# Performance work log

Hardware: AMD Instinct MI355X
Metric: run time of the kernel (lower is better)

The kernel has to match this reference:

```python
import jax, jax.numpy as jnp
import numpy as np

DN = ('NCDHW', 'DHWIO', 'NCDHW')


def _w(key, cin, cout):
    # kernel_size=3 in 3D, Minkowski-style fan-in scaling, no bias
    scale = 1.0 / np.sqrt(cin * 27)
    return jax.random.normal(key, (3, 3, 3, cin, cout), dtype=jnp.float32) * scale


def setup_inputs() -> dict:
    key = jax.random.key(0)
    ks = jax.random.split(key, 7)
    x = jax.random.normal(ks[0], (1, 1024, 4, 4, 4), dtype=jnp.float32)
    chans = [(1024, 512), (512, 256), (256, 128), (128, 64), (64, 32), (32, 1)]
    ws = {f'w{i+1}': _w(ks[i + 1], ci, co) for i, (ci, co) in enumerate(chans)}
    return {'x': x, **ws}


def _ct(x, w, stride):
    # conv-transpose, kernel 3, SAME padding: stride 2 doubles resolution,
    # stride 1 preserves it (dense analog of Minkowski generative transpose conv)
    return jax.lax.conv_transpose(x, w, strides=(stride, stride, stride),
                                  padding='SAME', dimension_numbers=DN)


def reference(x, w1, w2, w3, w4, w5, w6):
    h = jax.nn.relu(_ct(x, w1, 2))   # 1024 -> 512, 4^3 -> 8^3
    h = jax.nn.relu(_ct(h, w2, 1))   # 512 -> 256
    h = jax.nn.relu(_ct(h, w3, 2))   # 256 -> 128, 8^3 -> 16^3
    h = jax.nn.relu(_ct(h, w4, 1))   # 128 -> 64
    h = jax.nn.relu(_ct(h, w5, 2))   # 64 -> 32, 16^3 -> 32^3
    return _ct(h, w6, 1)             # 32 -> 1, no final ReLU
```

## Files before the change

kernel.cpp:

```cpp
#include <hip/hip_runtime.h>

typedef _Float16 half8 __attribute__((ext_vector_type(8)));
typedef _Float16 half4v __attribute__((ext_vector_type(4)));
typedef float floatx4 __attribute__((ext_vector_type(4)));


__global__ __launch_bounds__(256) void pad_x_k(const float* __restrict__ X,
                                               _Float16* __restrict__ P) {
  int idx = blockIdx.x * 256 + threadIdx.x;
  if (idx >= 125 * 1024) return;
  int c = idx & 1023;
  int r = idx >> 10;
  int px = r % 5, py = (r / 5) % 5, pz = r / 25;
  float v = 0.f;
  if (px >= 1 && py >= 1 && pz >= 1)
    v = X[c * 64 + (pz - 1) * 16 + (py - 1) * 4 + (px - 1)];
  P[idx] = (_Float16)v;
}

template <int S, int PS, int C, int RELU>
__global__ __launch_bounds__(256) void pad_k(const float* __restrict__ I,
                                             _Float16* __restrict__ P) {
  constexpr int TOT = PS * PS * PS * C;
  int idx = blockIdx.x * 256 + threadIdx.x;
  if (idx >= TOT) return;
  int c = idx % C;
  int r = idx / C;
  int px = r % PS;
  int ry = r / PS;
  int py = ry % PS, pz = ry / PS;
  int sx = px - 1, sy = py - 1, sz = pz - 1;
  float v = 0.f;
  if (sx >= 0 && sx < S && sy >= 0 && sy < S && sz >= 0 && sz < S) {
    v = I[(size_t)((sz * S + sy) * S + sx) * C + c];
    if (RELU) v = fmaxf(v, 0.f);
  }
  P[idx] = (_Float16)v;
}

__global__ __launch_bounds__(256) void wt_k(
    const float* __restrict__ w1, const float* __restrict__ w2,
    const float* __restrict__ w3, const float* __restrict__ w4,
    const float* __restrict__ w5, _Float16* __restrict__ t1,
    _Float16* __restrict__ t2, _Float16* __restrict__ t3,
    _Float16* __restrict__ t4, _Float16* __restrict__ t5) {
  int b = blockIdx.x;
  const float* W;
  _Float16* T;
  int cin, cout;
  if (b < 13824)      { W = w1; T = t1; cin = 1024; cout = 512; }
  else if (b < 17280) { b -= 13824; W = w2; T = t2; cin = 512; cout = 256; }
  else if (b < 18144) { b -= 17280; W = w3; T = t3; cin = 256; cout = 128; }
  else if (b < 18360) { b -= 18144; W = w4; T = t4; cin = 128; cout = 64; }
  else                { b -= 18360; W = w5; T = t5; cin = 64;  cout = 32; }
  const int citiles = cin >> 5;
  const int per_tap = (cout >> 5) * citiles;
  const int tap = b / per_tap;
  const int r = b - tap * per_tap;
  const int cot = r / citiles, cit = r - cot * citiles;

  __shared__ float tile[32][33];
  const int t = threadIdx.x;
  const int rr = t >> 3, c4 = (t & 7) * 4;
  const float* src =
      W + ((size_t)(tap * cin + cit * 32 + rr)) * cout + cot * 32 + c4;
  float4 v = *(const float4*)src;
  tile[rr][c4] = v.x; tile[rr][c4 + 1] = v.y;
  tile[rr][c4 + 2] = v.z; tile[rr][c4 + 3] = v.w;
  __syncthreads();
  half4v h;
  h[0] = (_Float16)tile[c4 + 0][rr];
  h[1] = (_Float16)tile[c4 + 1][rr];
  h[2] = (_Float16)tile[c4 + 2][rr];
  h[3] = (_Float16)tile[c4 + 3][rr];
  *(half4v*)(T + ((size_t)(tap * cout + cot * 32 + rr)) * cin + cit * 32 + c4) = h;
}

template <int CICHUNK, int CIN, int COUT, int NTILE, int STRIDE2, int SOUTU,
          int TZ, int PS, int USE_ATOMIC>
__global__ __launch_bounds__(256) void conv_mfma_k(
    const _Float16* __restrict__ P, const _Float16* __restrict__ Wt,
    float* __restrict__ O) {
  constexpr int M = TZ * 16;
  constexpr int MTZ = SOUTU / TZ;
  constexpr int MTXY = SOUTU / 4;
  constexpr int MT3 = MTZ * MTXY * MTXY;
  constexpr int KB = 32;
  constexpr int KP = KB + 8;
  constexpr int S = STRIDE2 ? 2 * SOUTU : SOUTU;

  __shared__ __align__(16) _Float16 As[M][KP];
  __shared__ __align__(16) _Float16 Bs[NTILE][KP];

  int bx = blockIdx.x;
  int cls = 0;
  if (STRIDE2) { cls = bx / MT3; bx -= cls * MT3; }
  const int clz = (cls >> 2) & 1, cly = (cls >> 1) & 1, clx = cls & 1;
  const int u0z = (bx / (MTXY * MTXY)) * TZ;
  const int u0y = ((bx / MTXY) % MTXY) * 4;
  const int u0x = (bx % MTXY) * 4;
  const int n_base = blockIdx.y * NTILE;
  const int ci_base = blockIdx.z * CICHUNK;

  const int t = threadIdx.x;
  const int lane = t & 63;
  const int wave = t >> 6;

  const int skq = t & 3;
  const int sp = t >> 2;
  const int spx = sp & 3, spy = (sp >> 2) & 3, spz = sp >> 4;
  const int aoff0 = ((spz * PS + spy) * PS + spx) * CIN;
  const int aoff1 = (((spz + 4) * PS + spy) * PS + spx) * CIN;

  const int m0w = (NTILE == 64) ? (wave >> 1) * 32 : wave * 32;
  const int n0w = (NTILE == 64) ? (wave & 1) * 32 : 0;
  const int fr = lane & 15;
  const int fq = lane >> 4;

  floatx4 acc[2][2];
#pragma unroll
  for (int i = 0; i < 2; i++)
#pragma unroll
    for (int j = 0; j < 2; j++) acc[i][j] = {0.f, 0.f, 0.f, 0.f};

  const int cz = STRIDE2 ? (clz ? 1 : 2) : 3;
  const int cy = STRIDE2 ? (cly ? 1 : 2) : 3;
  const int cx = STRIDE2 ? (clx ? 1 : 2) : 3;

  for (int iz = 0; iz < cz; iz++) {
    const int toz = STRIDE2 ? (clz ? 1 : iz) : iz;
    const int wz  = STRIDE2 ? (clz ? 1 : 2 * iz) : iz;
    for (int iy = 0; iy < cy; iy++) {
      const int toy = STRIDE2 ? (cly ? 1 : iy) : iy;
      const int wy  = STRIDE2 ? (cly ? 1 : 2 * iy) : iy;
      for (int ix = 0; ix < cx; ix++) {
        const int tox = STRIDE2 ? (clx ? 1 : ix) : ix;
        const int wx  = STRIDE2 ? (clx ? 1 : 2 * ix) : ix;
        const _Float16* Pb = P +
            (size_t)(((u0z + toz) * PS + (u0y + toy)) * PS + (u0x + tox)) * CIN +
            ci_base;
        const _Float16* Wb = Wt +
            ((size_t)((wz * 3 + wy) * 3 + wx) * COUT + n_base) * CIN + ci_base;
        for (int kb = 0; kb < CICHUNK / KB; kb++) {
          const int ko = kb * KB + skq * 8;
          *(half8*)&As[sp][skq * 8] = *(const half8*)(Pb + aoff0 + ko);
          if (M == 128)
            *(half8*)&As[sp + 64][skq * 8] = *(const half8*)(Pb + aoff1 + ko);
          if (NTILE == 64 || sp < NTILE)
            *(half8*)&Bs[sp][skq * 8] =
                *(const half8*)(Wb + (size_t)sp * CIN + ko);
          __syncthreads();
          half8 a0 = *(const half8*)&As[m0w + fr][fq * 8];
          half8 a1 = *(const half8*)&As[m0w + 16 + fr][fq * 8];
          half8 b0 = *(const half8*)&Bs[n0w + fr][fq * 8];
          half8 b1 = *(const half8*)&Bs[n0w + 16 + fr][fq * 8];
          acc[0][0] = __builtin_amdgcn_mfma_f32_16x16x32_f16(a0, b0, acc[0][0], 0, 0, 0);
          acc[0][1] = __builtin_amdgcn_mfma_f32_16x16x32_f16(a0, b1, acc[0][1], 0, 0, 0);
          acc[1][0] = __builtin_amdgcn_mfma_f32_16x16x32_f16(a1, b0, acc[1][0], 0, 0, 0);
          acc[1][1] = __builtin_amdgcn_mfma_f32_16x16x32_f16(a1, b1, acc[1][1], 0, 0, 0);
          __syncthreads();
        }
      }
    }
  }

#pragma unroll
  for (int i = 0; i < 2; i++) {
#pragma unroll
    for (int r = 0; r < 4; r++) {
      const int m = m0w + i * 16 + fq * 4 + r;
      const int mz = m >> 4, my = (m >> 2) & 3, mx = m & 3;
      int oz, oy, ox;
      if (STRIDE2) {
        oz = 2 * (u0z + mz) + clz;
        oy = 2 * (u0y + my) + cly;
        ox = 2 * (u0x + mx) + clx;
      } else {
        oz = u0z + mz;
        oy = u0y + my;
        ox = u0x + mx;
      }
      float* obase = O + (size_t)((oz * S + oy) * S + ox) * COUT + n_base + n0w;
#pragma unroll
      for (int j = 0; j < 2; j++) {
        float* o = obase + j * 16 + fr;
        if (USE_ATOMIC) atomicAdd(o, acc[i][j][r]);
        else *o = acc[i][j][r];
      }
    }
  }
}

__global__ __launch_bounds__(256) void conv6_k(const _Float16* __restrict__ P,
                                               const float* __restrict__ W6,
                                               float* __restrict__ O) {
  __shared__ __align__(16) float w[864];
  for (int i = threadIdx.x; i < 864; i += 256) w[i] = W6[i];
  __syncthreads();
  int idx = blockIdx.x * 256 + threadIdx.x;
  int x = idx & 31, y = (idx >> 5) & 31, z = idx >> 10;
  float a = 0.f;
  for (int dz = 0; dz < 3; dz++)
    for (int dy = 0; dy < 3; dy++)
      for (int dx = 0; dx < 3; dx++) {
        const _Float16* p =
            P + (size_t)(((z + dz) * 34 + (y + dy)) * 34 + (x + dx)) * 32;
        const float* ww = &w[((dz * 3 + dy) * 3 + dx) * 32];
#pragma unroll
        for (int c = 0; c < 32; c += 8) {
          half8 pv = *(const half8*)&p[c];
#pragma unroll
          for (int u = 0; u < 8; u++) a += (float)pv[u] * ww[c + u];
        }
      }
  O[idx] = a;
}

extern "C" void kernel_launch(void* const* d_in, const int* in_sizes, int n_in,
                              void* d_out, int out_size, void* d_ws,
                              size_t ws_size, hipStream_t stream) {
  const float* x  = (const float*)d_in[0];
  const float* w1 = (const float*)d_in[1];
  const float* w2 = (const float*)d_in[2];
  const float* w3 = (const float*)d_in[3];
  const float* w4 = (const float*)d_in[4];
  const float* w5 = (const float*)d_in[5];
  const float* w6 = (const float*)d_in[6];
  float* out = (float*)d_out;

  float* O1 = (float*)d_ws;
  float* O2 = O1 + 262144;
  float* O3 = O2 + 131072;
  float* O4 = O3 + 524288;
  float* O5 = O4 + 262144;
  _Float16* P1 = (_Float16*)(O5 + 1048576);
  _Float16* P2 = P1 + 128000;
  _Float16* P3 = P2 + 512000;
  _Float16* P4 = P3 + 186624;
  _Float16* P5 = P4 + 746496;
  _Float16* P6 = P5 + 314432;
  _Float16* T1 = P6 + 1257728;
  _Float16* T2 = T1 + 14155776;
  _Float16* T3 = T2 + 3538944;
  _Float16* T4 = T3 + 884736;
  _Float16* T5 = T4 + 221184;

  wt_k<<<18414, 256, 0, stream>>>(w1, w2, w3, w4, w5, T1, T2, T3, T4, T5);
  hipMemsetAsync(O1, 0, (262144 + 131072 + 524288 + 262144) * sizeof(float),
                 stream);

  pad_x_k<<<500, 256, 0, stream>>>(x, P1);
  conv_mfma_k<256, 1024, 512, 64, 1, 4, 4, 5, 1>
      <<<dim3(8, 8, 4), 256, 0, stream>>>(P1, T1, O1);
  pad_k<8, 10, 512, 1><<<2000, 256, 0, stream>>>(O1, P2);
  conv_mfma_k<64, 512, 256, 64, 0, 8, 4, 10, 1>
      <<<dim3(8, 4, 8), 256, 0, stream>>>(P2, T2, O2);
  pad_k<8, 9, 256, 1><<<729, 256, 0, stream>>>(O2, P3);
  conv_mfma_k<128, 256, 128, 64, 1, 8, 4, 9, 1>
      <<<dim3(64, 2, 2), 256, 0, stream>>>(P3, T3, O3);
  pad_k<16, 18, 128, 1><<<2916, 256, 0, stream>>>(O3, P4);
  conv_mfma_k<32, 128, 64, 64, 0, 16, 4, 18, 1>
      <<<dim3(64, 1, 4), 256, 0, stream>>>(P4, T4, O4);
  pad_k<16, 17, 64, 1><<<1229, 256, 0, stream>>>(O4, P5);
  conv_mfma_k<64, 64, 32, 32, 1, 16, 8, 17, 0>
      <<<dim3(256, 1, 1), 256, 0, stream>>>(P5, T5, O5);
  pad_k<32, 34, 32, 1><<<4913, 256, 0, stream>>>(O5, P6);
  conv6_k<<<128, 256, 0, stream>>>(P6, w6, out);

  (void)in_sizes; (void)n_in; (void)out_size; (void)ws_size;
}
```

Measured before the change: 238.2 us.

## Read fp32 weights directly in conv, prefetch next tile, fuse last pad

Drops the separate weight transpose/convert kernel. Each conv now loads fp32 weights in their original DHWIO layout straight from global memory and converts them to fp16 while writing shared memory. The main loop is flattened over taps and K-blocks with register double-buffering, so the next tile's loads overlap the current MFMA step. Layer 5 writes ReLU'd fp16 output directly into the padded buffer, removing one pad kernel. Split-K factors change for layers 1–3. The trade-off is reading fp32 weights, twice the bytes and with strided per-thread loads, and more atomics from the larger split-K.

```diff
diff --git a/kernel.cpp b/kernel.cpp
--- a/kernel.cpp
+++ b/kernel.cpp
@@ -38,56 +38,20 @@
   P[idx] = (_Float16)v;
 }
 
-__global__ __launch_bounds__(256) void wt_k(
-    const float* __restrict__ w1, const float* __restrict__ w2,
-    const float* __restrict__ w3, const float* __restrict__ w4,
-    const float* __restrict__ w5, _Float16* __restrict__ t1,
-    _Float16* __restrict__ t2, _Float16* __restrict__ t3,
-    _Float16* __restrict__ t4, _Float16* __restrict__ t5) {
-  int b = blockIdx.x;
-  const float* W;
-  _Float16* T;
-  int cin, cout;
-  if (b < 13824)      { W = w1; T = t1; cin = 1024; cout = 512; }
-  else if (b < 17280) { b -= 13824; W = w2; T = t2; cin = 512; cout = 256; }
-  else if (b < 18144) { b -= 17280; W = w3; T = t3; cin = 256; cout = 128; }
-  else if (b < 18360) { b -= 18144; W = w4; T = t4; cin = 128; cout = 64; }
-  else                { b -= 18360; W = w5; T = t5; cin = 64;  cout = 32; }
-  const int citiles = cin >> 5;
-  const int per_tap = (cout >> 5) * citiles;
-  const int tap = b / per_tap;
-  const int r = b - tap * per_tap;
-  const int cot = r / citiles, cit = r - cot * citiles;
-
-  __shared__ float tile[32][33];
-  const int t = threadIdx.x;
-  const int rr = t >> 3, c4 = (t & 7) * 4;
-  const float* src =
-      W + ((size_t)(tap * cin + cit * 32 + rr)) * cout + cot * 32 + c4;
-  float4 v = *(const float4*)src;
-  tile[rr][c4] = v.x; tile[rr][c4 + 1] = v.y;
-  tile[rr][c4 + 2] = v.z; tile[rr][c4 + 3] = v.w;
-  __syncthreads();
-  half4v h;
-  h[0] = (_Float16)tile[c4 + 0][rr];
-  h[1] = (_Float16)tile[c4 + 1][rr];
-  h[2] = (_Float16)tile[c4 + 2][rr];
-  h[3] = (_Float16)tile[c4 + 3][rr];
-  *(half4v*)(T + ((size_t)(tap * cout + cot * 32 + rr)) * cin + cit * 32 + c4) = h;
-}
-
 template <int CICHUNK, int CIN, int COUT, int NTILE, int STRIDE2, int SOUTU,
-          int TZ, int PS, int USE_ATOMIC>
+          int TZ, int PS, int STORE_MODE>
 __global__ __launch_bounds__(256) void conv_mfma_k(
-    const _Float16* __restrict__ P, const _Float16* __restrict__ Wt,
-    float* __restrict__ O) {
+    const _Float16* __restrict__ P, const float* __restrict__ W,
+    void* __restrict__ Optr) {
   constexpr int M = TZ * 16;
   constexpr int MTZ = SOUTU / TZ;
   constexpr int MTXY = SOUTU / 4;
   constexpr int MT3 = MTZ * MTXY * MTXY;
   constexpr int KB = 32;
-  constexpr int KP = KB + 8;
+  constexpr int KP = 40;
+  constexpr int KBI = CICHUNK / KB;
   constexpr int S = STRIDE2 ? 2 * SOUTU : SOUTU;
+  constexpr int BJ = (NTILE == 64) ? 8 : 4;
 
   __shared__ __align__(16) _Float16 As[M][KP];
   __shared__ __align__(16) _Float16 Bs[NTILE][KP];
@@ -109,59 +73,102 @@
   const int skq = t & 3;
   const int sp = t >> 2;
   const int spx = sp & 3, spy = (sp >> 2) & 3, spz = sp >> 4;
-  const int aoff0 = ((spz * PS + spy) * PS + spx) * CIN;
-  const int aoff1 = (((spz + 4) * PS + spy) * PS + spx) * CIN;
+  const int aoffsp = ((spz * PS + spy) * PS + spx) * CIN + skq * 8;
+  const int aoffsp2 = (((spz + 4) * PS + spy) * PS + spx) * CIN + skq * 8;
+
+  const int nB = t & (NTILE - 1);
+  const int k0B = (t / NTILE) * BJ;
 
   const int m0w = (NTILE == 64) ? (wave >> 1) * 32 : wave * 32;
   const int n0w = (NTILE == 64) ? (wave & 1) * 32 : 0;
   const int fr = lane & 15;
   const int fq = lane >> 4;
 
-  floatx4 acc[2][2];
-#pragma unroll
-  for (int i = 0; i < 2; i++)
-#pragma unroll
-    for (int j = 0; j < 2; j++) acc[i][j] = {0.f, 0.f, 0.f, 0.f};
-
   const int cz = STRIDE2 ? (clz ? 1 : 2) : 3;
   const int cy = STRIDE2 ? (cly ? 1 : 2) : 3;
   const int cx = STRIDE2 ? (clx ? 1 : 2) : 3;
-
-  for (int iz = 0; iz < cz; iz++) {
+  const int ctaps = cz * cy * cx;
+  const int NIT = ctaps * KBI;
+  const int shx = STRIDE2 ? (clx ? 0 : 1) : 0;
+  const int shy = STRIDE2 ? (cly ? 0 : 1) : 0;
+
+  floatx4 acc[2][2];
+#pragma unroll
+  for (int i = 0; i < 2; i++)
+#pragma unroll
+    for (int j = 0; j < 2; j++) acc[i][j] = {0.f, 0.f, 0.f, 0.f};
+
+  half8 raA = {}, raB = {}, raA2 = {}, raB2 = {};
+  float bwv[BJ] = {}, bwv2[BJ] = {};
+
+  auto load_it = [&](int it, half8& A0, half8& A1, float* BW) {
+    int tap, kb;
+    if (KBI == 1) { tap = it; kb = 0; }
+    else { tap = it / KBI; kb = it - tap * KBI; }
+    int iz, iy, ix;
+    if (STRIDE2) {
+      const int shyx = shx + shy;
+      iz = tap >> shyx;
+      int rem = tap - (iz << shyx);
+      iy = rem >> shx;
+      ix = rem - (iy << shx);
+    } else {
+      iz = tap / 9;
+      int rem = tap - iz * 9;
+      iy = rem / 3;
+      ix = rem - iy * 3;
+    }
     const int toz = STRIDE2 ? (clz ? 1 : iz) : iz;
     const int wz  = STRIDE2 ? (clz ? 1 : 2 * iz) : iz;
-    for (int iy = 0; iy < cy; iy++) {
-      const int toy = STRIDE2 ? (cly ? 1 : iy) : iy;
-      const int wy  = STRIDE2 ? (cly ? 1 : 2 * iy) : iy;
-      for (int ix = 0; ix < cx; ix++) {
-        const int tox = STRIDE2 ? (clx ? 1 : ix) : ix;
-        const int wx  = STRIDE2 ? (clx ? 1 : 2 * ix) : ix;
-        const _Float16* Pb = P +
-            (size_t)(((u0z + toz) * PS + (u0y + toy)) * PS + (u0x + tox)) * CIN +
-            ci_base;
-        const _Float16* Wb = Wt +
-            ((size_t)((wz * 3 + wy) * 3 + wx) * COUT + n_base) * CIN + ci_base;
-        for (int kb = 0; kb < CICHUNK / KB; kb++) {
-          const int ko = kb * KB + skq * 8;
-          *(half8*)&As[sp][skq * 8] = *(const half8*)(Pb + aoff0 + ko);
-          if (M == 128)
-            *(half8*)&As[sp + 64][skq * 8] = *(const half8*)(Pb + aoff1 + ko);
-          if (NTILE == 64 || sp < NTILE)
-            *(half8*)&Bs[sp][skq * 8] =
-                *(const half8*)(Wb + (size_t)sp * CIN + ko);
-          __syncthreads();
-          half8 a0 = *(const half8*)&As[m0w + fr][fq * 8];
-          half8 a1 = *(const half8*)&As[m0w + 16 + fr][fq * 8];
-          half8 b0 = *(const half8*)&Bs[n0w + fr][fq * 8];
-          half8 b1 = *(const half8*)&Bs[n0w + 16 + fr][fq * 8];
-          acc[0][0] = __builtin_amdgcn_mfma_f32_16x16x32_f16(a0, b0, acc[0][0], 0, 0, 0);
-          acc[0][1] = __builtin_amdgcn_mfma_f32_16x16x32_f16(a0, b1, acc[0][1], 0, 0, 0);
-          acc[1][0] = __builtin_amdgcn_mfma_f32_16x16x32_f16(a1, b0, acc[1][0], 0, 0, 0);
-          acc[1][1] = __builtin_amdgcn_mfma_f32_16x16x32_f16(a1, b1, acc[1][1], 0, 0, 0);
-          __syncthreads();
-        }
+    const int toy = STRIDE2 ? (cly ? 1 : iy) : iy;
+    const int wy  = STRIDE2 ? (cly ? 1 : 2 * iy) : iy;
+    const int tox = STRIDE2 ? (clx ? 1 : ix) : ix;
+    const int wx  = STRIDE2 ? (clx ? 1 : 2 * ix) : ix;
+    const int kofs = ci_base + kb * KB;
+    const size_t pbase =
+        (size_t)(((u0z + toz) * PS + (u0y + toy)) * PS + (u0x + tox)) * CIN +
+        kofs;
+    A0 = *(const half8*)(P + pbase + aoffsp);
+    if (M == 128) A1 = *(const half8*)(P + pbase + aoffsp2);
+    const int wtap = (wz * 3 + wy) * 3 + wx;
+    const float* wb =
+        W + ((size_t)wtap * CIN + kofs + k0B) * COUT + n_base + nB;
+#pragma unroll
+    for (int j = 0; j < BJ; j++) BW[j] = wb[(size_t)j * COUT];
+  };
+
+  load_it(0, raA, raB, bwv);
+
+  for (int it = 0; it < NIT; ++it) {
+    *(half8*)&As[sp][skq * 8] = raA;
+    if (M == 128) *(half8*)&As[sp + 64][skq * 8] = raB;
+    {
+      half4v h0;
+#pragma unroll
+      for (int j = 0; j < 4; j++) h0[j] = (_Float16)bwv[j];
+      *(half4v*)&Bs[nB][k0B] = h0;
+      if (BJ == 8) {
+        half4v h1;
+#pragma unroll
+        for (int j = 0; j < 4; j++) h1[j] = (_Float16)bwv[4 + j];
+        *(half4v*)&Bs[nB][k0B + 4] = h1;
       }
     }
+    __syncthreads();
+    if (it + 1 < NIT) load_it(it + 1, raA2, raB2, bwv2);
+    half8 a0 = *(const half8*)&As[m0w + fr][fq * 8];
+    half8 a1 = *(const half8*)&As[m0w + 16 + fr][fq * 8];
+    half8 b0 = *(const half8*)&Bs[n0w + fr][fq * 8];
+    half8 b1 = *(const half8*)&Bs[n0w + 16 + fr][fq * 8];
+    acc[0][0] = __builtin_amdgcn_mfma_f32_16x16x32_f16(a0, b0, acc[0][0], 0, 0, 0);
+    acc[0][1] = __builtin_amdgcn_mfma_f32_16x16x32_f16(a0, b1, acc[0][1], 0, 0, 0);
+    acc[1][0] = __builtin_amdgcn_mfma_f32_16x16x32_f16(a1, b0, acc[1][0], 0, 0, 0);
+    acc[1][1] = __builtin_amdgcn_mfma_f32_16x16x32_f16(a1, b1, acc[1][1], 0, 0, 0);
+    __syncthreads();
+    raA = raA2;
+    raB = raB2;
+#pragma unroll
+    for (int j = 0; j < BJ; j++) bwv[j] = bwv2[j];
   }
 
 #pragma unroll
@@ -180,12 +187,21 @@
         oy = u0y + my;
         ox = u0x + mx;
       }
-      float* obase = O + (size_t)((oz * S + oy) * S + ox) * COUT + n_base + n0w;
-#pragma unroll
-      for (int j = 0; j < 2; j++) {
-        float* o = obase + j * 16 + fr;
-        if (USE_ATOMIC) atomicAdd(o, acc[i][j][r]);
-        else *o = acc[i][j][r];
+      if (STORE_MODE == 2) {
+        _Float16* o = (_Float16*)Optr +
+            (size_t)(((oz + 1) * (S + 2) + (oy + 1)) * (S + 2) + (ox + 1)) *
+                COUT + n_base + n0w;
+#pragma unroll
+        for (int j = 0; j < 2; j++)
+          o[j * 16 + fr] = (_Float16)fmaxf(acc[i][j][r], 0.f);
+      } else {
+        float* o = (float*)Optr +
+            (size_t)((oz * S + oy) * S + ox) * COUT + n_base + n0w;
+#pragma unroll
+        for (int j = 0; j < 2; j++) {
+          if (STORE_MODE == 1) atomicAdd(o + j * 16 + fr, acc[i][j][r]);
+          else o[j * 16 + fr] = acc[i][j][r];
+        }
       }
     }
   }
@@ -232,39 +248,31 @@
   float* O2 = O1 + 262144;
   float* O3 = O2 + 131072;
   float* O4 = O3 + 524288;
-  float* O5 = O4 + 262144;
-  _Float16* P1 = (_Float16*)(O5 + 1048576);
+  _Float16* P6 = (_Float16*)(O4 + 262144);
+  _Float16* P1 = P6 + 1257728;
   _Float16* P2 = P1 + 128000;
   _Float16* P3 = P2 + 512000;
   _Float16* P4 = P3 + 186624;
   _Float16* P5 = P4 + 746496;
-  _Float16* P6 = P5 + 314432;
-  _Float16* T1 = P6 + 1257728;
-  _Float16* T2 = T1 + 14155776;
-  _Float16* T3 = T2 + 3538944;
-  _Float16* T4 = T3 + 884736;
-  _Float16* T5 = T4 + 221184;
-
-  wt_k<<<18414, 256, 0, stream>>>(w1, w2, w3, w4, w5, T1, T2, T3, T4, T5);
-  hipMemsetAsync(O1, 0, (262144 + 131072 + 524288 + 262144) * sizeof(float),
+
+  hipMemsetAsync(d_ws, 0, 1179648 * sizeof(float) + 1257728 * sizeof(_Float16),
                  stream);
 
   pad_x_k<<<500, 256, 0, stream>>>(x, P1);
-  conv_mfma_k<256, 1024, 512, 64, 1, 4, 4, 5, 1>
-      <<<dim3(8, 8, 4), 256, 0, stream>>>(P1, T1, O1);
+  conv_mfma_k<128, 1024, 512, 64, 1, 4, 4, 5, 1>
+      <<<dim3(8, 8, 8), 256, 0, stream>>>(P1, w1, O1);
   pad_k<8, 10, 512, 1><<<2000, 256, 0, stream>>>(O1, P2);
-  conv_mfma_k<64, 512, 256, 64, 0, 8, 4, 10, 1>
-      <<<dim3(8, 4, 8), 256, 0, stream>>>(P2, T2, O2);
+  conv_mfma_k<32, 512, 256, 64, 0, 8, 4, 10, 1>
+      <<<dim3(8, 4, 16), 256, 0, stream>>>(P2, w2, O2);
   pad_k<8, 9, 256, 1><<<729, 256, 0, stream>>>(O2, P3);
-  conv_mfma_k<128, 256, 128, 64, 1, 8, 4, 9, 1>
-      <<<dim3(64, 2, 2), 256, 0, stream>>>(P3, T3, O3);
+  conv_mfma_k<64, 256, 128, 64, 1, 8, 4, 9, 1>
+      <<<dim3(64, 2, 4), 256, 0, stream>>>(P3, w3, O3);
   pad_k<16, 18, 128, 1><<<2916, 256, 0, stream>>>(O3, P4);
   conv_mfma_k<32, 128, 64, 64, 0, 16, 4, 18, 1>
-      <<<dim3(64, 1, 4), 256, 0, stream>>>(P4, T4, O4);
+      <<<dim3(64, 1, 4), 256, 0, stream>>>(P4, w4, O4);
   pad_k<16, 17, 64, 1><<<1229, 256, 0, stream>>>(O4, P5);
-  conv_mfma_k<64, 64, 32, 32, 1, 16, 8, 17, 0>
-      <<<dim3(256, 1, 1), 256, 0, stream>>>(P5, T5, O5);
-  pad_k<32, 34, 32, 1><<<4913, 256, 0, stream>>>(O5, P6);
+  conv_mfma_k<64, 64, 32, 32, 1, 16, 8, 17, 2>
+      <<<dim3(256, 1, 1), 256, 0, stream>>>(P5, w5, P6);
   conv6_k<<<128, 256, 0, stream>>>(P6, w6, out);
 
   (void)in_sizes; (void)n_in; (void)out_size; (void)ws_size;
```

Measured after the change: 216.1 us. -9.3%, faster.
